# Performance work log

Measured on AMD Instinct MI355X. Metric: run time of the kernel, lower is better.

## Reference

```python
import jax, jax.numpy as jnp
import numpy as np

B, C, H, W, N_REF = 4, 256, 128, 128, 4


def setup_inputs() -> dict:
    key = jax.random.key(0)
    ks = jax.random.split(key, 9)
    s = 1.0 / np.sqrt(C)
    x = jax.random.normal(ks[0], (B, C, H, W), jnp.float32)
    Wq = jax.random.normal(ks[1], (C, C), jnp.float32) * s
    bq = jax.random.normal(ks[2], (C,), jnp.float32) * 0.01
    Wk = jax.random.normal(ks[3], (C, C), jnp.float32) * s
    bk = jax.random.normal(ks[4], (C,), jnp.float32) * 0.01
    Wv = jax.random.normal(ks[5], (C, C), jnp.float32) * s
    bv = jax.random.normal(ks[6], (C,), jnp.float32) * 0.01
    Wo = jax.random.normal(ks[7], (2 * N_REF, C), jnp.float32) * s
    bo = jax.random.normal(ks[8], (2 * N_REF,), jnp.float32) * 0.01
    return {"x": x, "Wq": Wq, "bq": bq, "Wk": Wk, "bk": bk,
            "Wv": Wv, "bv": bv, "Wo": Wo, "bo": bo}


def _proj(Wt, bt, x):
    # 1x1 conv == per-pixel channel matmul
    return jnp.einsum('oc,bchw->bohw', Wt, x) + bt[None, :, None, None]


def reference(x, Wq, bq, Wk, bk, Wv, bv, Wo, bo):
    b, c, h, w = x.shape
    n = Wo.shape[0] // 2
    hw = h * w

    Q = _proj(Wq, bq, x)
    K = _proj(Wk, bk, x)
    V = _proj(Wv, bv, x)

    offsets = _proj(Wo, bo, Q).reshape(b, n, 2, h, w)

    grid_w = jnp.arange(w, dtype=jnp.float32)[None, None, None, :]
    grid_h = jnp.arange(h, dtype=jnp.float32)[None, None, :, None]
    # clamp then truncate toward zero (matches torch .clamp().long() for >=0 values)
    ref_w = jnp.clip(grid_w + offsets[:, :, 0], 0, w - 1)
    ref_h = jnp.clip(grid_h + offsets[:, :, 1], 0, h - 1)
    idx = (jax.lax.stop_gradient(ref_h).astype(jnp.int32) * w
           + jax.lax.stop_gradient(ref_w).astype(jnp.int32)).reshape(b, n * hw)

    K_flat = K.reshape(b, c, hw)
    V_flat = V.reshape(b, c, hw)
    Kg = jnp.take_along_axis(K_flat, idx[:, None, :], axis=2).reshape(b, c, n, hw)
    Vg = jnp.take_along_axis(V_flat, idx[:, None, :], axis=2).reshape(b, c, n, hw)

    Q_flat = Q.reshape(b, c, hw)
    # NOTE: original module applies no softmax/scale — raw dot-product weights
    attn = jnp.einsum('bch,bcnh->bnh', Q_flat, Kg)
    out = jnp.einsum('bnh,bcnh->bch', attn, Vg)
    return out.reshape(b, c, h, w)
```

## Files before the change

kernel.cpp:

```cpp
#include <hip/hip_runtime.h>

#define HW   16384
#define CH   256
#define WD   128
#define NPTS 4

typedef _Float16 half8 __attribute__((ext_vector_type(8)));
typedef _Float16 half4 __attribute__((ext_vector_type(4)));
typedef float    f32x4 __attribute__((ext_vector_type(4)));

#define WS_XT    0ull
#define WS_WQK   33554432ull
#define WS_WV    33685504ull
#define WS_WOQ   33816576ull
#define WS_BOF   33824768ull
#define WS_CVEC  33824832ull
#define WS_DVEC  33825856ull
#define WS_SC    33826880ull
#define WS_SVEC  33826944ull
#define WS_IDX   34089088ull

__global__ void k_wprep(const float* __restrict__ Wq, const float* __restrict__ bq,
                        const float* __restrict__ Wk, const float* __restrict__ bk,
                        const float* __restrict__ Wv, const float* __restrict__ bv,
                        const float* __restrict__ Wo, const float* __restrict__ bo,
                        _Float16* __restrict__ wqk16, float* __restrict__ cvec,
                        _Float16* __restrict__ wv16, float* __restrict__ woq,
                        float* __restrict__ bof, float* __restrict__ dvec,
                        float* __restrict__ scst) {
    int bid = blockIdx.x, t = threadIdx.x;
    if (bid < 256) {
        int i = bid;
        float s = 0.f;
        for (int o = 0; o < 256; o++) s += Wk[o * 256 + i] * Wq[o * 256 + t];
        wqk16[i * 256 + t] = (_Float16)s;
        if (t == 0) {
            float cs = 0.f;
            for (int o = 0; o < 256; o++) cs += Wk[o * 256 + i] * bq[o];
            cvec[i] = cs;
        }
    } else if (bid < 512) {
        int r = bid - 256;
        wv16[r * 256 + t] = (_Float16)Wv[r * 256 + t];
    } else if (bid < 520) {
        int j = bid - 512;
        float s = 0.f;
        for (int o = 0; o < 256; o++) s += Wo[j * 256 + o] * Wq[o * 256 + t];
        woq[t * 8 + j] = s;
        if (t == 0) {
            float tt = bo[j];
            for (int o = 0; o < 256; o++) tt += Wo[j * 256 + o] * bq[o];
            bof[j] = tt;
        }
    } else {
        float s = 0.f;
        for (int o = 0; o < 256; o++) s += bk[o] * Wq[o * 256 + t];
        dvec[t] = s;
        if (t == 0) {
            float sc = 0.f;
            for (int o = 0; o < 256; o++) sc += bq[o] * bk[o];
            scst[0] = sc;
        }
    }
}

__launch_bounds__(256)
__global__ void k_prep(const float* __restrict__ x, const float* __restrict__ woq,
                       const float* __restrict__ bof, const float* __restrict__ dvec,
                       const float* __restrict__ scst,
                       _Float16* __restrict__ xt, int* __restrict__ idxb,
                       float* __restrict__ svec) {
    __shared__ float    wl[256 * 8];
    __shared__ float    dl[256];
    __shared__ float    bl8[8];
    __shared__ _Float16 tile[64][280];
    __shared__ float    red[4][64][8];
    __shared__ float    reds[4][64];

    int t = threadIdx.x;
    for (int i = t; i < 256 * 8; i += 256) wl[i] = woq[i];
    dl[t] = dvec[t];
    if (t < 8) bl8[t] = bof[t];
    __syncthreads();

    int b = blockIdx.y;
    int p0 = blockIdx.x * 64;
    int pl = t & 63, cg = t >> 6;
    const float* xb = x + (size_t)b * CH * HW + p0 + pl;

    float acc[8];
    #pragma unroll
    for (int j = 0; j < 8; j++) acc[j] = 0.f;
    float accs = 0.f;

    for (int i0 = 0; i0 < 64; i0 += 8) {
        half8 hv;
        #pragma unroll
        for (int i = 0; i < 8; i++) {
            int c = cg * 64 + i0 + i;
            float xv = xb[(size_t)c * HW];
            hv[i] = (_Float16)xv;
            accs += dl[c] * xv;
            #pragma unroll
            for (int j = 0; j < 8; j++) acc[j] += wl[c * 8 + j] * xv;
        }
        *(half8*)(&tile[pl][cg * 64 + i0]) = hv;
    }
    #pragma unroll
    for (int j = 0; j < 8; j++) red[cg][pl][j] = acc[j];
    reds[cg][pl] = accs;
    __syncthreads();

    {
        int n = cg, p = p0 + pl;
        float sw_ = bl8[2 * n]     + red[0][pl][2 * n]     + red[1][pl][2 * n]
                                   + red[2][pl][2 * n]     + red[3][pl][2 * n];
        float sh_ = bl8[2 * n + 1] + red[0][pl][2 * n + 1] + red[1][pl][2 * n + 1]
                                   + red[2][pl][2 * n + 1] + red[3][pl][2 * n + 1];
        int h = p >> 7, w = p & 127;
        float rw = fminf(fmaxf((float)w + sw_, 0.f), 127.f);
        float rh = fminf(fmaxf((float)h + sh_, 0.f), 127.f);
        idxb[(b * NPTS + n) * HW + p] = ((int)rh) * WD + (int)rw;
        if (cg == 0)
            svec[b * HW + p] = reds[0][pl] + reds[1][pl] + reds[2][pl] + reds[3][pl] + scst[0];
    }

    {
        int row = t >> 2;
        size_t gbase = ((size_t)(b * HW + p0 + row)) * 256;
        #pragma unroll
        for (int s = 0; s < 8; s++) {
            int seg = (t & 3) + s * 4;
            *(uint4*)(xt + gbase + seg * 8) = *(const uint4*)(&tile[row][seg * 8]);
        }
    }
}

__launch_bounds__(512, 4)
__global__ void k_fused(const _Float16* __restrict__ xt, const _Float16* __restrict__ wqk16,
                        const _Float16* __restrict__ wv16, const float* __restrict__ cvec,
                        const float* __restrict__ bv, const int* __restrict__ idxb,
                        const float* __restrict__ svec, float* __restrict__ out) {
    __shared__ _Float16 AQW[64 * 256];
    __shared__ _Float16 Bs[2][256 * 32];
    __shared__ float    asf[64];

    int tid = threadIdx.x;
    int b = blockIdx.y;
    int bx = blockIdx.x;
    int logical = (bx & 7) * 32 + (bx >> 3);
    int p0 = logical * 64;
    size_t mrow0 = (size_t)b * HW + p0;

    int lane = tid & 63, wid = tid >> 6;
    int wr = wid >> 2, wc = wid & 3;
    int g = lane >> 4, r = lane & 15;

    {
        int row = tid >> 3;
        int c0 = tid & 7;
        const uint4* src = (const uint4*)(xt + (mrow0 + row) * 256);
        #pragma unroll
        for (int s = 0; s < 4; s++) {
            int c8 = c0 + s * 8;
            uint4 v = src[c8];
            *(uint4*)(&AQW[(row << 8) + 8 * (c8 ^ (row & 7))]) = v;
        }
    }

    int brow = tid >> 1, bseg = tid & 1;
    int bslot0 = (bseg * 2)     ^ ((brow >> 1) & 3);
    int bslot1 = (bseg * 2 + 1) ^ ((brow >> 1) & 3);
    uint4 br0, br1;

    {
        const _Float16* p = wqk16 + (size_t)brow * 256 + bseg * 16;
        br0 = *(const uint4*)(p);
        br1 = *(const uint4*)(p + 8);
        *(uint4*)(&Bs[0][brow * 32 + bslot0 * 8]) = br0;
        *(uint4*)(&Bs[0][brow * 32 + bslot1 * 8]) = br1;
        p += 32;
        br0 = *(const uint4*)(p);
        br1 = *(const uint4*)(p + 8);
    }
    __syncthreads();

    f32x4 acc[2][4] = {};
    #pragma unroll
    for (int kt = 0; kt < 8; kt++) {
        if (kt < 7) {
            _Float16* B = &Bs[(kt + 1) & 1][0];
            *(uint4*)(&B[brow * 32 + bslot0 * 8]) = br0;
            *(uint4*)(&B[brow * 32 + bslot1 * 8]) = br1;
        }
        if (kt < 6) {
            const _Float16* p = wqk16 + (size_t)brow * 256 + (kt + 2) * 32 + bseg * 16;
            br0 = *(const uint4*)(p);
            br1 = *(const uint4*)(p + 8);
        }
        half8 af[2], bf[4];
        #pragma unroll
        for (int mb = 0; mb < 2; mb++) {
            int row = wr * 32 + mb * 16 + r;
            af[mb] = *(const half8*)(&AQW[(row << 8) + ((kt * 32 + g * 8) ^ ((row & 7) << 3))]);
        }
        #pragma unroll
        for (int nb = 0; nb < 4; nb++) {
            int row = wc * 64 + nb * 16 + r;
            bf[nb] = *(const half8*)(&Bs[kt & 1][row * 32 + ((g ^ ((row >> 1) & 3)) << 3)]);
        }
        #pragma unroll
        for (int mb = 0; mb < 2; mb++)
            #pragma unroll
            for (int nb = 0; nb < 4; nb++)
                acc[mb][nb] = __builtin_amdgcn_mfma_f32_16x16x32_f16(bf[nb], af[mb], acc[mb][nb], 0, 0, 0);
        __syncthreads();
    }

    #pragma unroll
    for (int mb = 0; mb < 2; mb++) {
        int row = wr * 32 + mb * 16 + r;
        #pragma unroll
        for (int nb = 0; nb < 4; nb++) {
            int ncol = wc * 64 + nb * 16 + g * 4;
            f32x4 cv = *(const f32x4*)(cvec + ncol);
            half4 h;
            #pragma unroll
            for (int i = 0; i < 4; i++) h[i] = (_Float16)(acc[mb][nb][i] + cv[i]);
            *(half4*)(&AQW[(row << 8) + (ncol ^ ((row & 7) << 3))]) = h;
        }
    }
    __syncthreads();

    {
        int seg = tid & 15, pslot = tid >> 4;
        #pragma unroll
        for (int it = 0; it < 2; it++) {
            int pl = it * 32 + pslot;
            size_t m = mrow0 + pl;
            int qa0 = (pl << 8) + ((seg * 8)       ^ ((pl & 7) << 3));
            int qa1 = (pl << 8) + ((128 + seg * 8) ^ ((pl & 7) << 3));
            half8 q0 = *(const half8*)(&AQW[qa0]);
            half8 q1 = *(const half8*)(&AQW[qa1]);
            float sv = svec[m];
            int jj[NPTS];
            #pragma unroll
            for (int n = 0; n < NPTS; n++) jj[n] = idxb[(b * NPTS + n) * HW + p0 + pl];

            half8 xv0[NPTS], xv1[NPTS];
            #pragma unroll
            for (int n = 0; n < NPTS; n++) {
                const _Float16* xr = xt + ((size_t)b * HW + jj[n]) * 256;
                xv0[n] = *(const half8*)(xr + seg * 8);
                xv1[n] = *(const half8*)(xr + 128 + seg * 8);
            }
            float o0[8], o1[8];
            #pragma unroll
            for (int e = 0; e < 8; e++) { o0[e] = 0.f; o1[e] = 0.f; }
            float asl = 0.f;
            #pragma unroll
            for (int n = 0; n < NPTS; n++) {
                float d = 0.f;
                #pragma unroll
                for (int e = 0; e < 8; e++) d += (float)q0[e] * (float)xv0[n][e];
                #pragma unroll
                for (int e = 0; e < 8; e++) d += (float)q1[e] * (float)xv1[n][e];
                d += __shfl_xor(d, 1);
                d += __shfl_xor(d, 2);
                d += __shfl_xor(d, 4);
                d += __shfl_xor(d, 8);
                float a = d + sv;
                asl += a;
                #pragma unroll
                for (int e = 0; e < 8; e++) o0[e] += a * (float)xv0[n][e];
                #pragma unroll
                for (int e = 0; e < 8; e++) o1[e] += a * (float)xv1[n][e];
            }
            half8 h0, h1;
            #pragma unroll
            for (int e = 0; e < 8; e++) { h0[e] = (_Float16)o0[e]; h1[e] = (_Float16)o1[e]; }
            *(half8*)(&AQW[qa0]) = h0;
            *(half8*)(&AQW[qa1]) = h1;
            if (seg == 0) asf[pl] = asl;
        }
    }

    {
        const _Float16* p = wv16 + (size_t)brow * 256 + bseg * 16;
        br0 = *(const uint4*)(p);
        br1 = *(const uint4*)(p + 8);
        *(uint4*)(&Bs[0][brow * 32 + bslot0 * 8]) = br0;
        *(uint4*)(&Bs[0][brow * 32 + bslot1 * 8]) = br1;
        p += 32;
        br0 = *(const uint4*)(p);
        br1 = *(const uint4*)(p + 8);
    }
    __syncthreads();

    f32x4 acc2[2][4] = {};
    #pragma unroll
    for (int kt = 0; kt < 8; kt++) {
        if (kt < 7) {
            _Float16* B = &Bs[(kt + 1) & 1][0];
            *(uint4*)(&B[brow * 32 + bslot0 * 8]) = br0;
            *(uint4*)(&B[brow * 32 + bslot1 * 8]) = br1;
        }
        if (kt < 6) {
            const _Float16* p = wv16 + (size_t)brow * 256 + (kt + 2) * 32 + bseg * 16;
            br0 = *(const uint4*)(p);
            br1 = *(const uint4*)(p + 8);
        }
        half8 af[2], bf[4];
        #pragma unroll
        for (int mb = 0; mb < 2; mb++) {
            int row = wr * 32 + mb * 16 + r;
            af[mb] = *(const half8*)(&AQW[(row << 8) + ((kt * 32 + g * 8) ^ ((row & 7) << 3))]);
        }
        #pragma unroll
        for (int nb = 0; nb < 4; nb++) {
            int row = wc * 64 + nb * 16 + r;
            bf[nb] = *(const half8*)(&Bs[kt & 1][row * 32 + ((g ^ ((row >> 1) & 3)) << 3)]);
        }
        #pragma unroll
        for (int mb = 0; mb < 2; mb++)
            #pragma unroll
            for (int nb = 0; nb < 4; nb++)
                acc2[mb][nb] = __builtin_amdgcn_mfma_f32_16x16x32_f16(bf[nb], af[mb], acc2[mb][nb], 0, 0, 0);
        __syncthreads();
    }

    #pragma unroll
    for (int mb = 0; mb < 2; mb++) {
        int mrow = wr * 32 + mb * 16 + r;
        float am = asf[mrow];
        float* obase = out + (size_t)b * CH * HW + p0 + mrow;
        #pragma unroll
        for (int nb = 0; nb < 4; nb++) {
            int cb = wc * 64 + nb * 16 + g * 4;
            f32x4 bb = *(const f32x4*)(bv + cb);
            #pragma unroll
            for (int i = 0; i < 4; i++)
                obase[(size_t)(cb + i) * HW] = acc2[mb][nb][i] + am * bb[i];
        }
    }
}

extern "C" void kernel_launch(void* const* d_in, const int* in_sizes, int n_in,
                              void* d_out, int out_size, void* d_ws, size_t ws_size,
                              hipStream_t stream) {
    const float* x  = (const float*)d_in[0];
    const float* Wq = (const float*)d_in[1];
    const float* bq = (const float*)d_in[2];
    const float* Wk = (const float*)d_in[3];
    const float* bk = (const float*)d_in[4];
    const float* Wv = (const float*)d_in[5];
    const float* bv = (const float*)d_in[6];
    const float* Wo = (const float*)d_in[7];
    const float* bo = (const float*)d_in[8];
    (void)in_sizes; (void)n_in; (void)out_size; (void)ws_size;

    char* ws = (char*)d_ws;
    _Float16* xt    = (_Float16*)(ws + WS_XT);
    _Float16* wqk16 = (_Float16*)(ws + WS_WQK);
    _Float16* wv16  = (_Float16*)(ws + WS_WV);
    float*    woq   = (float*)(ws + WS_WOQ);
    float*    bof   = (float*)(ws + WS_BOF);
    float*    cvec  = (float*)(ws + WS_CVEC);
    float*    dvec  = (float*)(ws + WS_DVEC);
    float*    scst  = (float*)(ws + WS_SC);
    float*    svec  = (float*)(ws + WS_SVEC);
    int*      idxb  = (int*)(ws + WS_IDX);

    k_wprep<<<521, 256, 0, stream>>>(Wq, bq, Wk, bk, Wv, bv, Wo, bo,
                                     wqk16, cvec, wv16, woq, bof, dvec, scst);
    k_prep<<<dim3(256, 4), 256, 0, stream>>>(x, woq, bof, dvec, scst, xt, idxb, svec);
    k_fused<<<dim3(256, 4), 512, 0, stream>>>(xt, wqk16, wv16, cvec, bv, idxb, svec,
                                              (float*)d_out);
}
```

Baseline: 90.17 us.

## Halve fused kernel block to 256 threads with 4x4 MFMA tiles per wave

Reduces the fused kernel block from 8 waves to 4 waves. Each wave now covers all 64 pixel rows and 64 output channels (4x4 MFMA tiles) instead of 32x64. Loads of the A tile and the weight tiles are rearranged so each thread moves more data, and the gather loop runs more iterations per thread. The aim is more work per wave and better reuse of A fragments, at the cost of higher register pressure and fewer waves to hide latency.

```diff
diff --git a/kernel.cpp b/kernel.cpp
--- a/kernel.cpp
+++ b/kernel.cpp
@@ -136,7 +136,7 @@
     }
 }
 
-__launch_bounds__(512, 4)
+__launch_bounds__(256, 2)
 __global__ void k_fused(const _Float16* __restrict__ xt, const _Float16* __restrict__ wqk16,
                         const _Float16* __restrict__ wv16, const float* __restrict__ cvec,
                         const float* __restrict__ bv, const int* __restrict__ idxb,
@@ -152,65 +152,62 @@
     int p0 = logical * 64;
     size_t mrow0 = (size_t)b * HW + p0;
 
-    int lane = tid & 63, wid = tid >> 6;
-    int wr = wid >> 2, wc = wid & 3;
+    int lane = tid & 63, w = tid >> 6;
     int g = lane >> 4, r = lane & 15;
 
     {
-        int row = tid >> 3;
-        int c0 = tid & 7;
-        const uint4* src = (const uint4*)(xt + (mrow0 + row) * 256);
+        int arow = tid >> 2, ac0 = tid & 3;
+        const uint4* asrc = (const uint4*)(xt + (mrow0 + arow) * 256);
+        #pragma unroll
+        for (int s = 0; s < 8; s++) {
+            int c8 = ac0 + s * 4;
+            uint4 v = asrc[c8];
+            *(uint4*)(&AQW[(arow << 8) + 8 * (c8 ^ (arow & 7))]) = v;
+        }
+    }
+
+    int brow = tid;
+    uint4 br[4];
+
+    {
+        const uint4* p = (const uint4*)(wqk16 + (size_t)brow * 256);
         #pragma unroll
         for (int s = 0; s < 4; s++) {
-            int c8 = c0 + s * 8;
-            uint4 v = src[c8];
-            *(uint4*)(&AQW[(row << 8) + 8 * (c8 ^ (row & 7))]) = v;
-        }
-    }
-
-    int brow = tid >> 1, bseg = tid & 1;
-    int bslot0 = (bseg * 2)     ^ ((brow >> 1) & 3);
-    int bslot1 = (bseg * 2 + 1) ^ ((brow >> 1) & 3);
-    uint4 br0, br1;
-
-    {
-        const _Float16* p = wqk16 + (size_t)brow * 256 + bseg * 16;
-        br0 = *(const uint4*)(p);
-        br1 = *(const uint4*)(p + 8);
-        *(uint4*)(&Bs[0][brow * 32 + bslot0 * 8]) = br0;
-        *(uint4*)(&Bs[0][brow * 32 + bslot1 * 8]) = br1;
-        p += 32;
-        br0 = *(const uint4*)(p);
-        br1 = *(const uint4*)(p + 8);
-    }
-    __syncthreads();
-
-    f32x4 acc[2][4] = {};
+            uint4 v = p[s];
+            *(uint4*)(&Bs[0][brow * 32 + 8 * (s ^ ((brow >> 1) & 3))]) = v;
+        }
+        #pragma unroll
+        for (int s = 0; s < 4; s++) br[s] = p[4 + s];
+    }
+    __syncthreads();
+
+    f32x4 acc[4][4] = {};
     #pragma unroll
     for (int kt = 0; kt < 8; kt++) {
         if (kt < 7) {
             _Float16* B = &Bs[(kt + 1) & 1][0];
-            *(uint4*)(&B[brow * 32 + bslot0 * 8]) = br0;
-            *(uint4*)(&B[brow * 32 + bslot1 * 8]) = br1;
+            #pragma unroll
+            for (int s = 0; s < 4; s++)
+                *(uint4*)(&B[brow * 32 + 8 * (s ^ ((brow >> 1) & 3))]) = br[s];
         }
         if (kt < 6) {
-            const _Float16* p = wqk16 + (size_t)brow * 256 + (kt + 2) * 32 + bseg * 16;
-            br0 = *(const uint4*)(p);
-            br1 = *(const uint4*)(p + 8);
-        }
-        half8 af[2], bf[4];
-        #pragma unroll
-        for (int mb = 0; mb < 2; mb++) {
-            int row = wr * 32 + mb * 16 + r;
+            const uint4* p = (const uint4*)(wqk16 + (size_t)brow * 256 + (kt + 2) * 32);
+            #pragma unroll
+            for (int s = 0; s < 4; s++) br[s] = p[s];
+        }
+        half8 af[4], bf[4];
+        #pragma unroll
+        for (int mb = 0; mb < 4; mb++) {
+            int row = mb * 16 + r;
             af[mb] = *(const half8*)(&AQW[(row << 8) + ((kt * 32 + g * 8) ^ ((row & 7) << 3))]);
         }
         #pragma unroll
         for (int nb = 0; nb < 4; nb++) {
-            int row = wc * 64 + nb * 16 + r;
-            bf[nb] = *(const half8*)(&Bs[kt & 1][row * 32 + ((g ^ ((row >> 1) & 3)) << 3)]);
-        }
-        #pragma unroll
-        for (int mb = 0; mb < 2; mb++)
+            int row = w * 64 + nb * 16 + r;
+            bf[nb] = *(const half8*)(&Bs[kt & 1][row * 32 + 8 * (g ^ ((row >> 1) & 3))]);
+        }
+        #pragma unroll
+        for (int mb = 0; mb < 4; mb++)
             #pragma unroll
             for (int nb = 0; nb < 4; nb++)
                 acc[mb][nb] = __builtin_amdgcn_mfma_f32_16x16x32_f16(bf[nb], af[mb], acc[mb][nb], 0, 0, 0);
@@ -218,11 +215,11 @@
     }
 
     #pragma unroll
-    for (int mb = 0; mb < 2; mb++) {
-        int row = wr * 32 + mb * 16 + r;
+    for (int mb = 0; mb < 4; mb++) {
+        int row = mb * 16 + r;
         #pragma unroll
         for (int nb = 0; nb < 4; nb++) {
-            int ncol = wc * 64 + nb * 16 + g * 4;
+            int ncol = w * 64 + nb * 16 + g * 4;
             f32x4 cv = *(const f32x4*)(cvec + ncol);
             half4 h;
             #pragma unroll
@@ -235,8 +232,8 @@
     {
         int seg = tid & 15, pslot = tid >> 4;
         #pragma unroll
-        for (int it = 0; it < 2; it++) {
-            int pl = it * 32 + pslot;
+        for (int it = 0; it < 4; it++) {
+            int pl = it * 16 + pslot;
             size_t m = mrow0 + pl;
             int qa0 = (pl << 8) + ((seg * 8)       ^ ((pl & 7) << 3));
             int qa1 = (pl << 8) + ((128 + seg * 8) ^ ((pl & 7) << 3));
@@ -286,43 +283,44 @@
     }
 
     {
-        const _Float16* p = wv16 + (size_t)brow * 256 + bseg * 16;
-        br0 = *(const uint4*)(p);
-        br1 = *(const uint4*)(p + 8);
-        *(uint4*)(&Bs[0][brow * 32 + bslot0 * 8]) = br0;
-        *(uint4*)(&Bs[0][brow * 32 + bslot1 * 8]) = br1;
-        p += 32;
-        br0 = *(const uint4*)(p);
-        br1 = *(const uint4*)(p + 8);
-    }
-    __syncthreads();
-
-    f32x4 acc2[2][4] = {};
+        const uint4* p = (const uint4*)(wv16 + (size_t)brow * 256);
+        #pragma unroll
+        for (int s = 0; s < 4; s++) {
+            uint4 v = p[s];
+            *(uint4*)(&Bs[0][brow * 32 + 8 * (s ^ ((brow >> 1) & 3))]) = v;
+        }
+        #pragma unroll
+        for (int s = 0; s < 4; s++) br[s] = p[4 + s];
+    }
+    __syncthreads();
+
+    f32x4 acc2[4][4] = {};
     #pragma unroll
     for (int kt = 0; kt < 8; kt++) {
         if (kt < 7) {
             _Float16* B = &Bs[(kt + 1) & 1][0];
-            *(uint4*)(&B[brow * 32 + bslot0 * 8]) = br0;
-            *(uint4*)(&B[brow * 32 + bslot1 * 8]) = br1;
+            #pragma unroll
+            for (int s = 0; s < 4; s++)
+                *(uint4*)(&B[brow * 32 + 8 * (s ^ ((brow >> 1) & 3))]) = br[s];
         }
         if (kt < 6) {
-            const _Float16* p = wv16 + (size_t)brow * 256 + (kt + 2) * 32 + bseg * 16;
-            br0 = *(const uint4*)(p);
-            br1 = *(const uint4*)(p + 8);
-        }
-        half8 af[2], bf[4];
-        #pragma unroll
-        for (int mb = 0; mb < 2; mb++) {
-            int row = wr * 32 + mb * 16 + r;
+            const uint4* p = (const uint4*)(wv16 + (size_t)brow * 256 + (kt + 2) * 32);
+            #pragma unroll
+            for (int s = 0; s < 4; s++) br[s] = p[s];
+        }
+        half8 af[4], bf[4];
+        #pragma unroll
+        for (int mb = 0; mb < 4; mb++) {
+            int row = mb * 16 + r;
             af[mb] = *(const half8*)(&AQW[(row << 8) + ((kt * 32 + g * 8) ^ ((row & 7) << 3))]);
         }
         #pragma unroll
         for (int nb = 0; nb < 4; nb++) {
-            int row = wc * 64 + nb * 16 + r;
-            bf[nb] = *(const half8*)(&Bs[kt & 1][row * 32 + ((g ^ ((row >> 1) & 3)) << 3)]);
-        }
-        #pragma unroll
-        for (int mb = 0; mb < 2; mb++)
+            int row = w * 64 + nb * 16 + r;
+            bf[nb] = *(const half8*)(&Bs[kt & 1][row * 32 + 8 * (g ^ ((row >> 1) & 3))]);
+        }
+        #pragma unroll
+        for (int mb = 0; mb < 4; mb++)
             #pragma unroll
             for (int nb = 0; nb < 4; nb++)
                 acc2[mb][nb] = __builtin_amdgcn_mfma_f32_16x16x32_f16(bf[nb], af[mb], acc2[mb][nb], 0, 0, 0);
@@ -330,13 +328,13 @@
     }
 
     #pragma unroll
-    for (int mb = 0; mb < 2; mb++) {
-        int mrow = wr * 32 + mb * 16 + r;
+    for (int mb = 0; mb < 4; mb++) {
+        int mrow = mb * 16 + r;
         float am = asf[mrow];
         float* obase = out + (size_t)b * CH * HW + p0 + mrow;
         #pragma unroll
         for (int nb = 0; nb < 4; nb++) {
-            int cb = wc * 64 + nb * 16 + g * 4;
+            int cb = w * 64 + nb * 16 + g * 4;
             f32x4 bb = *(const f32x4*)(bv + cb);
             #pragma unroll
             for (int i = 0; i < 4; i++)
@@ -374,6 +372,6 @@
     k_wprep<<<521, 256, 0, stream>>>(Wq, bq, Wk, bk, Wv, bv, Wo, bo,
                                      wqk16, cvec, wv16, woq, bof, dvec, scst);
     k_prep<<<dim3(256, 4), 256, 0, stream>>>(x, woq, bof, dvec, scst, xt, idxb, svec);
-    k_fused<<<dim3(256, 4), 512, 0, stream>>>(xt, wqk16, wv16, cvec, bv, idxb, svec,
+    k_fused<<<dim3(256, 4), 256, 0, stream>>>(xt, wqk16, wv16, cvec, bv, idxb, svec,
                                               (float*)d_out);
 }
```

Measured after the change: 138.7 us. 53.9% more time.
